# Performance work log

Hardware: AMD Instinct MI355X
Metric: run time of the kernel (lower is better)

The kernel has to match this reference:

```python
import jax, jax.numpy as jnp
import numpy as np

B, D, R = 256, 4096, 16
MAX_R = 2 * R - 1  # static upper bound on radius; per-row steps masked by r_mask


def setup_inputs() -> dict:
    key = jax.random.key(0)
    kx, kw, kb = jax.random.split(key, 3)
    x = (jax.random.uniform(kx, (B, D)) < 0.5).astype(jnp.float32)  # random bits
    A = jax.random.normal(kw, (D, D), dtype=jnp.float32) * 0.01
    W = (A + A.T) * 0.5  # symmetric quadratic coupling
    bias = jax.random.normal(kb, (D,), dtype=jnp.float32) * 0.1
    return {"x": x, "W": W, "bias": bias}


def reference(x, W, bias):
    # energy model: score(x) = 0.5 * x' W x + b' x  (per batch row)
    score_fn = lambda z: 0.5 * jnp.einsum('bd,de,be->b', z, W, z) + z @ bias
    grad_fn = jax.grad(lambda z: score_fn(z).sum())

    key = jax.random.key(42)
    k_rad, k_samp, k_acc = jax.random.split(key, 3)
    radius = jax.random.randint(k_rad, (B, 1), 1, 2 * R)
    r_mask = (jnp.arange(MAX_R)[None, :] < radius).astype(x.dtype)  # [B, MAX_R]

    score_x = score_fn(x)                                  # [B]
    grad_x = jax.lax.stop_gradient(grad_fn(x))             # detach as in torch
    score_change_x = (1.0 - 2.0 * x) * grad_x * 0.5        # [B, D] proposal logits

    b_idx = jnp.arange(B)

    def body(carry, inp):
        cur_x, blocked = carry
        k, m = inp  # per-step RNG key, per-step mask column [B]
        idx = jax.random.categorical(k, score_change_x + blocked)  # multinomial w/ zeroed probs
        cur_bits = cur_x[b_idx, idx]
        cur_x = cur_x.at[b_idx, idx].set(m * (1.0 - cur_bits) + (1.0 - m) * cur_bits)
        blocked = blocked.at[b_idx, idx].set(-jnp.inf)  # prob_x[b, idx] = 0
        return (cur_x, blocked), idx

    keys = jax.random.split(k_samp, MAX_R)
    (y, _), idx_steps = jax.lax.scan(body, (x, jnp.zeros_like(x)), (keys, r_mask.T))
    idx_all = idx_steps.T  # [B, MAX_R]

    score_y = score_fn(y)
    grad_y = jax.lax.stop_gradient(grad_fn(y))
    score_change_y = (1.0 - 2.0 * y) * grad_y * 0.5

    # masked log-softmax tensors: step j's proposal excludes indices flipped at other steps
    oh = jax.nn.one_hot(idx_all, D, dtype=x.dtype)        # [B, MAX_R, D]
    cum = jnp.cumsum(oh, axis=1)
    before = cum - oh                                      # indices sampled at steps i < j
    after = cum[:, -1:, :] - cum                           # indices sampled at steps i > j
    change_fwd = jnp.where(before > 0, -jnp.inf, score_change_x[:, None, :])
    change_bwd = jnp.where(after > 0, -jnp.inf, score_change_y[:, None, :])

    g_fwd = jnp.take_along_axis(jax.nn.log_softmax(change_fwd, axis=-1), idx_all[:, :, None], axis=2)[..., 0]
    g_bwd = jnp.take_along_axis(jax.nn.log_softmax(change_bwd, axis=-1), idx_all[:, :, None], axis=2)[..., 0]
    log_fwd = jnp.sum(g_fwd * r_mask, axis=-1) + score_x
    log_bwd = jnp.sum(g_bwd * r_mask, axis=-1) + score_y

    log_acc = log_bwd - log_fwd
    u = jax.random.uniform(k_acc, (B,))
    accepted = (jnp.exp(log_acc) >= u).astype(x.dtype)[:, None]  # [B, 1]
    y_sg = jax.lax.stop_gradient(y)
    acc_sg = jax.lax.stop_gradient(accepted)
    return y_sg * acc_sg + (1.0 - acc_sg) * x
```

## Files before the change

### kernel.cpp

```cpp
#include <hip/hip_runtime.h>
#include <math.h>

#define BB 256
#define DD 4096
#define MAXR 31
#define NCAND 4
#define CAPG 192
#define U_THRESH 0.9778f
#define GUARD 4.0f

typedef unsigned short u16;
typedef u16 u16x4 __attribute__((ext_vector_type(4)));
typedef u16 u16x8 __attribute__((ext_vector_type(8)));
typedef __bf16 bf16x8 __attribute__((ext_vector_type(8)));
typedef float f32x16 __attribute__((ext_vector_type(16)));

__device__ __forceinline__ void tf2x32(unsigned k0, unsigned k1, unsigned c0, unsigned c1,
                                       unsigned &o0, unsigned &o1) {
  unsigned ks2 = k0 ^ k1 ^ 0x1BD11BDAu;
  unsigned x0 = c0 + k0;
  unsigned x1 = c1 + k1;
#define TF_ROT(v, r) (((v) << (r)) | ((v) >> (32 - (r))))
#define TF_R(r) { x0 += x1; x1 = TF_ROT(x1, r); x1 ^= x0; }
  TF_R(13) TF_R(15) TF_R(26) TF_R(6)   x0 += k1;  x1 += ks2 + 1u;
  TF_R(17) TF_R(29) TF_R(16) TF_R(24)  x0 += ks2; x1 += k0 + 2u;
  TF_R(13) TF_R(15) TF_R(26) TF_R(6)   x0 += k0;  x1 += k1 + 3u;
  TF_R(17) TF_R(29) TF_R(16) TF_R(24)  x0 += k1;  x1 += ks2 + 4u;
  TF_R(13) TF_R(15) TF_R(26) TF_R(6)   x0 += ks2; x1 += k0 + 5u;
#undef TF_R
#undef TF_ROT
  o0 = x0; o1 = x1;
}

__device__ __forceinline__ unsigned tf_xor(unsigned k0, unsigned k1, unsigned c0, unsigned c1) {
  unsigned a, b; tf2x32(k0, k1, c0, c1, a, b); return a ^ b;
}

__device__ __forceinline__ float bits_to_unit(unsigned bits) {
  return __uint_as_float(0x3f800000u | (bits >> 9)) - 1.0f;
}

__device__ __forceinline__ void keys_of(int j, unsigned &kk0, unsigned &kk1) {
  unsigned ks0, ks1;
  tf2x32(0u, 42u, 0u, 1u, ks0, ks1);
  tf2x32(ks0, ks1, 0u, (unsigned)j, kk0, kk1);
}

__device__ __forceinline__ int radius_of(int b) {
  unsigned krad0, krad1, k10, k11, k20, k21;
  tf2x32(0u, 42u, 0u, 0u, krad0, krad1);
  tf2x32(krad0, krad1, 0u, 0u, k10, k11);
  tf2x32(krad0, krad1, 0u, 1u, k20, k21);
  unsigned hi = tf_xor(k10, k11, 0u, (unsigned)b);
  unsigned lo = tf_xor(k20, k21, 0u, (unsigned)b);
  return 1 + (int)(((hi % 31u) * 4u + (lo % 31u)) % 31u);
}

__device__ __forceinline__ float uacc_of(int b) {
  unsigned ka0, ka1;
  tf2x32(0u, 42u, 0u, 2u, ka0, ka1);
  return bits_to_unit(tf_xor(ka0, ka1, 0u, (unsigned)b));
}

__device__ __forceinline__ double dlog(double x) {
  unsigned long long ub = (unsigned long long)__double_as_longlong(x);
  int e = (int)((ub >> 52) & 0x7FFull) - 1022;
  double m = __longlong_as_double((long long)((ub & 0x000FFFFFFFFFFFFFull) | 0x3FE0000000000000ull));
  if (m < 0.70710678118654752440) { m *= 2.0; e -= 1; }
  double r = (m - 1.0) / (m + 1.0);
  double z = r * r;
  double s = fma(z, fma(z, fma(z, fma(z, fma(z, fma(z, 1.0/15.0, 1.0/13.0),
                1.0/11.0), 1.0/9.0), 1.0/7.0), 1.0/5.0), 1.0/3.0);
  double t2 = 2.0 * r;
  return fma((double)e, 0.69314718055994530942, fma(t2 * z, s, t2));
}

__device__ __forceinline__ float gumbel_from_u(float f) {
  float uu = (f == 0.0f) ? 1.17549435e-38f : f;
  float t1 = (float)dlog((double)uu);
  return -(float)dlog((double)(-t1));
}

__device__ __forceinline__ float gumbel_of(unsigned kk0, unsigned kk1, unsigned n) {
  return gumbel_from_u(bits_to_unit(tf_xor(kk0, kk1, 0u, n)));
}

__device__ __forceinline__ double blockReduce1024(double v, double* lds) {
  int t = threadIdx.x;
  #pragma unroll
  for (int off = 32; off > 0; off >>= 1) v += __shfl_down(v, off);
  __syncthreads();
  if ((t & 63) == 0) lds[t >> 6] = v;
  __syncthreads();
  double s = 0.0;
  #pragma unroll
  for (int i = 0; i < 16; i++) s += lds[i];
  return s;
}

__device__ __forceinline__ void split3(float w, u16 &h, u16 &l, u16 &q) {
  __bf16 hb = (__bf16)w;
  float r = w - (float)hb;
  __bf16 lb = (__bf16)r;
  float r2 = r - (float)lb;
  __bf16 qb = (__bf16)r2;
  h = __builtin_bit_cast(u16, hb);
  l = __builtin_bit_cast(u16, lb);
  q = __builtin_bit_cast(u16, qb);
}

__global__ __launch_bounds__(256, 2) void k_mega(
    const float* __restrict__ x, const float* __restrict__ W,
    float* __restrict__ Cpart, int klen, int ngemm,
    u16* __restrict__ flt_list, int* __restrict__ flt_cnt) {
  int t = threadIdx.x;

  if ((int)blockIdx.x < ngemm) {
    int g = blockIdx.x;
    int nt = g & 63, mt = (g >> 6) & 1, kc = g >> 7;
    int k0 = kc * klen;

    __shared__ alignas(16) u16 As[4][128][8];
    __shared__ alignas(16) u16 Bs[3][4][64][8];

    const float* xrow = x + (size_t)(mt * 128) * DD + k0;
    const float* wrow = W + (size_t)(nt * 64) * DD + k0;

    int am = t >> 2, akg = t & 3;
    int bn = t >> 2, bkg = t & 3;

    float4 aR0, aR1, aR2, aR3;
    float4 bR0, bR1;
    int nsteps = klen / 32;

    {
      const float* ap = xrow + (size_t)am * DD + akg * 8;
      aR0 = *(const float4*)ap;       aR1 = *(const float4*)(ap + 4);
      const float* ap2 = ap + (size_t)64 * DD;
      aR2 = *(const float4*)ap2;      aR3 = *(const float4*)(ap2 + 4);
      const float* wp = wrow + (size_t)bn * DD + bkg * 8;
      bR0 = *(const float4*)wp;       bR1 = *(const float4*)(wp + 4);
    }

    int wid = t >> 6, lane = t & 63;
    int wr = (wid >> 1) * 64, wc = (wid & 1) * 32;
    int lm = lane & 31, lh = lane >> 5;

    f32x16 acc[2];
    #pragma unroll
    for (int i = 0; i < 2; i++)
      #pragma unroll
      for (int r = 0; r < 16; r++) acc[i][r] = 0.0f;

    for (int s = 0; s < nsteps; s++) {
      __syncthreads();
      {
        float af32[8];
        *(float4*)&af32[0] = aR0; *(float4*)&af32[4] = aR1;
        u16x8 av;
        #pragma unroll
        for (int i = 0; i < 8; i++) av[i] = __builtin_bit_cast(u16, (__bf16)af32[i]);
        *(u16x8*)&As[akg][am][0] = av;
        *(float4*)&af32[0] = aR2; *(float4*)&af32[4] = aR3;
        #pragma unroll
        for (int i = 0; i < 8; i++) av[i] = __builtin_bit_cast(u16, (__bf16)af32[i]);
        *(u16x8*)&As[akg][am + 64][0] = av;
      }
      {
        float wv[8];
        *(float4*)&wv[0] = bR0; *(float4*)&wv[4] = bR1;
        u16x8 ph, pl, pq;
        #pragma unroll
        for (int i = 0; i < 8; i++) {
          u16 hh, ll, qq;
          split3(wv[i], hh, ll, qq);
          ph[i] = hh; pl[i] = ll; pq[i] = qq;
        }
        *(u16x8*)&Bs[0][bkg][bn][0] = ph;
        *(u16x8*)&Bs[1][bkg][bn][0] = pl;
        *(u16x8*)&Bs[2][bkg][bn][0] = pq;
      }
      __syncthreads();
      if (s + 1 < nsteps) {
        int kk = (s + 1) * 32;
        const float* ap = xrow + (size_t)am * DD + kk + akg * 8;
        aR0 = *(const float4*)ap;       aR1 = *(const float4*)(ap + 4);
        const float* ap2 = ap + (size_t)64 * DD;
        aR2 = *(const float4*)ap2;      aR3 = *(const float4*)(ap2 + 4);
        const float* wp = wrow + (size_t)bn * DD + kk + bkg * 8;
        bR0 = *(const float4*)wp;       bR1 = *(const float4*)(wp + 4);
      }
      bf16x8 af[2][2];
      #pragma unroll
      for (int mf = 0; mf < 2; mf++)
        #pragma unroll
        for (int h = 0; h < 2; h++)
          af[mf][h] = *(const bf16x8*)&As[2 * h + lh][wr + mf * 32 + lm][0];
      __builtin_amdgcn_s_setprio(1);
      #pragma unroll
      for (int p = 0; p < 3; p++) {
        bf16x8 b0 = *(const bf16x8*)&Bs[p][lh][wc + lm][0];
        bf16x8 b1 = *(const bf16x8*)&Bs[p][2 + lh][wc + lm][0];
        #pragma unroll
        for (int mf = 0; mf < 2; mf++) {
          acc[mf] = __builtin_amdgcn_mfma_f32_32x32x16_bf16(af[mf][0], b0, acc[mf], 0, 0, 0);
          acc[mf] = __builtin_amdgcn_mfma_f32_32x32x16_bf16(af[mf][1], b1, acc[mf], 0, 0, 0);
        }
      }
      __builtin_amdgcn_s_setprio(0);
    }

    float* Cp = Cpart + (size_t)kc * ((size_t)BB * DD);
    #pragma unroll
    for (int mf = 0; mf < 2; mf++) {
      int col   = nt * 64 + wc + lm;
      int rbase = mt * 128 + wr + mf * 32 + 4 * lh;
      #pragma unroll
      for (int r = 0; r < 16; r++) {
        int row = rbase + (r & 3) + 8 * (r >> 2);
        Cp[(size_t)row * DD + col] = acc[mf][r];
      }
    }
  } else {
    int fb = (int)blockIdx.x - ngemm;
    int b = fb / MAXR, j = fb % MAXR;
    unsigned kk0, kk1;
    keys_of(j, kk0, kk1);
    unsigned base = (unsigned)(b * DD);

    __shared__ int fcnt;
    __shared__ u16 fl[CAPG];
    if (t == 0) fcnt = 0;
    __syncthreads();

    #pragma unroll
    for (int p = 0; p < 16; p++) {
      int d = t + 256*p;
      unsigned bits = tf_xor(kk0, kk1, 0u, base + (unsigned)d);
      float f = bits_to_unit(bits);
      if (f >= U_THRESH) {
        int pos = atomicAdd(&fcnt, 1);
        if (pos < CAPG) fl[pos] = (u16)d;
      }
    }
    __syncthreads();
    int n = fcnt;
    if (t == 0) flt_cnt[fb] = n;
    int nstore = n < CAPG ? n : CAPG;
    if (t < nstore) flt_list[(size_t)fb * CAPG + t] = fl[t];
  }
}

__global__ __launch_bounds__(1024) void k_redscore(
    const float* __restrict__ Cpart, const float* __restrict__ bias,
    const float* __restrict__ x, float* __restrict__ grad, float* __restrict__ sc,
    double* __restrict__ score, float* __restrict__ scmax, int KS) {
  int b = blockIdx.x, t = threadIdx.x;
  int d0 = t * 4;
  size_t o = (size_t)b * DD + d0;
  float a0 = 0.f, a1 = 0.f, a2 = 0.f, a3 = 0.f;
  for (int kc = 0; kc < KS; kc++) {
    float4 c = *(const float4*)&Cpart[(size_t)kc * BB * DD + o];
    a0 += c.x; a1 += c.y; a2 += c.z; a3 += c.w;
  }
  float4 bv = *(const float4*)&bias[d0];
  float4 xv = *(const float4*)&x[o];
  float gg[4] = { a0 + bv.x, a1 + bv.y, a2 + bv.z, a3 + bv.w };
  float xx[4] = { xv.x, xv.y, xv.z, xv.w };
  float bb[4] = { bv.x, bv.y, bv.z, bv.w };
  *(float4*)&grad[o] = *(float4*)&gg[0];
  float scv[4];
  double s1 = 0.0, s2 = 0.0;
  float mx = -INFINITY;
  #pragma unroll
  for (int k = 0; k < 4; k++) {
    scv[k] = (1.0f - 2.0f * xx[k]) * gg[k] * 0.5f;
    mx = fmaxf(mx, scv[k]);
    s1 += (double)xx[k] * (double)gg[k];
    s2 += (double)xx[k] * (double)bb[k];
  }
  *(float4*)&sc[o] = *(float4*)&scv[0];
  __shared__ double lds[16];
  double S1 = blockReduce1024(s1, lds);
  double S2 = blockReduce1024(s2, lds);
  #pragma unroll
  for (int off = 32; off > 0; off >>= 1) mx = fmaxf(mx, __shfl_down(mx, off));
  __shared__ float lmx[16];
  __syncthreads();
  if ((t & 63) == 0) lmx[t >> 6] = mx;
  __syncthreads();
  if (t == 0) {
    float m = lmx[0];
    #pragma unroll
    for (int i = 1; i < 16; i++) m = fmaxf(m, lmx[i]);
    score[b] = 0.5 * (S1 + S2);
    scmax[b] = m;
  }
}

__global__ __launch_bounds__(256) void k_topk(const float* __restrict__ sc_x,
                                              const float* __restrict__ scmax,
                                              const u16* __restrict__ flt_list,
                                              const int* __restrict__ flt_cnt,
                                              int* __restrict__ cand_i) {
  int fb = blockIdx.x;
  int b = fb / MAXR, j = fb % MAXR;
  unsigned kk0, kk1;
  keys_of(j, kk0, kk1);
  int t = threadIdx.x;
  unsigned base = (unsigned)(b * DD);

  __shared__ float win_v_s;
  __shared__ int   win_i_s;
  __shared__ float ls_v[4];
  __shared__ int   ls_i[4];

  int n = flt_cnt[fb];
  bool need_fallback = (n > CAPG) || (n < NCAND);

  if (!need_fallback) {
    float v; int di;
    if (t < n) {
      int d = (int)flt_list[(size_t)fb * CAPG + t];
      float f = bits_to_unit(tf_xor(kk0, kk1, 0u, base + (unsigned)d));
      v = sc_x[(size_t)b*DD + d] + gumbel_from_u(f);
      di = d;
    } else { v = -INFINITY; di = 0x7FFFFFFF; }
    bool dead = (t >= n);
    float v4 = -INFINITY;
    for (int r = 0; r < NCAND; r++) {
      float bv = dead ? -INFINITY : v;
      int   bi = dead ? 0x7FFFFFFF : di;
      #pragma unroll
      for (int off = 32; off > 0; off >>= 1) {
        float ov = __shfl_down(bv, off);
        int   oi = __shfl_down(bi, off);
        if (ov > bv || (ov == bv && oi < bi)) { bv = ov; bi = oi; }
      }
      if ((t & 63) == 0) { ls_v[t >> 6] = bv; ls_i[t >> 6] = bi; }
      __syncthreads();
      if (t == 0) {
        float fv = ls_v[0]; int fi = ls_i[0];
        #pragma unroll
        for (int w = 1; w < 4; w++)
          if (ls_v[w] > fv || (ls_v[w] == fv && ls_i[w] < fi)) { fv = ls_v[w]; fi = ls_i[w]; }
        win_v_s = fv; win_i_s = fi;
        cand_i[(size_t)fb * NCAND + r] = fi;
      }
      __syncthreads();
      v4 = win_v_s;
      if (di == win_i_s) dead = true;
    }
    if (v4 >= scmax[b] + GUARD) return;
    need_fallback = true;
    __syncthreads();
  }

  {
    float v[16];
    #pragma unroll
    for (int p = 0; p < 16; p++) {
      int d = t + 256*p;
      v[p] = sc_x[(size_t)b*DD + d] + gumbel_of(kk0, kk1, base + (unsigned)d);
    }
    unsigned alive = 0xFFFFu;
    float lv = -INFINITY; int li = 0x7FFFFFFF;
    #pragma unroll
    for (int p = 0; p < 16; p++)
      if (v[p] > lv) { lv = v[p]; li = t + 256*p; }
    for (int r = 0; r < NCAND; r++) {
      float bv = lv; int bi = li;
      #pragma unroll
      for (int off = 32; off > 0; off >>= 1) {
        float ov = __shfl_down(bv, off);
        int   oi = __shfl_down(bi, off);
        if (ov > bv || (ov == bv && oi < bi)) { bv = ov; bi = oi; }
      }
      if ((t & 63) == 0) { ls_v[t >> 6] = bv; ls_i[t >> 6] = bi; }
      __syncthreads();
      if (t == 0) {
        float fv = ls_v[0]; int fi = ls_i[0];
        #pragma unroll
        for (int w = 1; w < 4; w++)
          if (ls_v[w] > fv || (ls_v[w] == fv && ls_i[w] < fi)) { fv = ls_v[w]; fi = ls_i[w]; }
        win_i_s = fi;
        cand_i[(size_t)fb * NCAND + r] = fi;
      }
      __syncthreads();
      if (r < NCAND - 1) {
        int wi = win_i_s;
        if (t == (wi & 255)) {
          alive &= ~(1u << (wi >> 8));
          lv = -INFINITY; li = 0x7FFFFFFF;
          #pragma unroll
          for (int p = 0; p < 16; p++)
            if (((alive >> p) & 1u) && v[p] > lv) { lv = v[p]; li = t + 256*p; }
        }
      }
    }
  }
}

__global__ __launch_bounds__(1024) void k_sely(
    const int* __restrict__ cand_i, const float* __restrict__ sc_x,
    const float* __restrict__ x, const float* __restrict__ W,
    const float* __restrict__ bias, const float* __restrict__ grad_x,
    int* __restrict__ idx_all, float* __restrict__ yv, float* __restrict__ sc_y,
    double* __restrict__ score_y) {
  int b = blockIdx.x, t = threadIdx.x;
  __shared__ unsigned mask[128];
  __shared__ int cl[MAXR * NCAND];
  __shared__ int fidx[MAXR];
  __shared__ float fsgn[MAXR];
  __shared__ int jfail_s;
  __shared__ int nf_s;
  __shared__ float ls_v[16];
  __shared__ int   ls_i[16];
  if (t < 128) mask[t] = 0u;
  if (t < MAXR * NCAND) cl[t] = cand_i[(size_t)b * MAXR * NCAND + t];
  if (t == 0) nf_s = radius_of(b);
  __syncthreads();

  int jdone = 0;
  while (true) {
    if (t == 0) {
      int j = jdone;
      while (j < MAXR) {
        int pick = -1;
        #pragma unroll
        for (int r = 0; r < NCAND; r++) {
          int idx = cl[j * NCAND + r];
          if (pick < 0 && !((mask[idx >> 5] >> (idx & 31)) & 1u)) pick = idx;
        }
        if (pick < 0) break;
        fidx[j] = pick;
        idx_all[b * MAXR + j] = pick;
        mask[pick >> 5] |= (1u << (pick & 31));
        j++;
      }
      jfail_s = j;
    }
    __syncthreads();
    int jf = jfail_s;
    if (jf >= MAXR) break;
    {
      unsigned kk0, kk1;
      keys_of(jf, kk0, kk1);
      float lv = -INFINITY; int li = 0x7FFFFFFF;
      #pragma unroll
      for (int q = 0; q < 4; q++) {
        int d = t * 4 + q;
        if ((mask[d >> 5] >> (d & 31)) & 1u) continue;
        float vv = sc_x[(size_t)b*DD + d] + gumbel_of(kk0, kk1, (unsigned)(b*DD + d));
        if (vv > lv || (vv == lv && d < li)) { lv = vv; li = d; }
      }
      #pragma unroll
      for (int off = 32; off > 0; off >>= 1) {
        float ov = __shfl_down(lv, off);
        int   oi = __shfl_down(li, off);
        if (ov > lv || (ov == lv && oi < li)) { lv = ov; li = oi; }
      }
      if ((t & 63) == 0) { ls_v[t >> 6] = lv; ls_i[t >> 6] = li; }
      __syncthreads();
      if (t == 0) {
        float fv = ls_v[0]; int fi = ls_i[0];
        #pragma unroll
        for (int w = 1; w < 16; w++)
          if (ls_v[w] > fv || (ls_v[w] == fv && ls_i[w] < fi)) { fv = ls_v[w]; fi = ls_i[w]; }
        fidx[jf] = fi;
        idx_all[b * MAXR + jf] = fi;
        mask[fi >> 5] |= (1u << (fi & 31));
      }
      __syncthreads();
    }
    jdone = jf + 1;
  }

  int nf = nf_s;
  if (t < nf) fsgn[t] = 1.0f - 2.0f * x[(size_t)b*DD + fidx[t]];
  __syncthreads();

  int d0 = t * 4;
  size_t o = (size_t)b * DD + d0;
  float4 gv4 = *(const float4*)&grad_x[o];
  float4 xv4 = *(const float4*)&x[o];
  float4 bv4 = *(const float4*)&bias[d0];
  float g[4]  = { gv4.x, gv4.y, gv4.z, gv4.w };
  float xx[4] = { xv4.x, xv4.y, xv4.z, xv4.w };
  float yy[4] = { xv4.x, xv4.y, xv4.z, xv4.w };
  for (int jj = 0; jj < nf; jj++) {
    int fd = fidx[jj];
    float s = fsgn[jj];
    float4 wv = *(const float4*)&W[(size_t)fd * DD + d0];
    g[0] = fmaf(s, wv.x, g[0]);
    g[1] = fmaf(s, wv.y, g[1]);
    g[2] = fmaf(s, wv.z, g[2]);
    g[3] = fmaf(s, wv.w, g[3]);
    int r = fd - d0;
    if (r >= 0 && r < 4) yy[r] = 1.0f - xx[r];
  }
  float scy[4];
  double s1 = 0.0, s2 = 0.0;
  float bb[4] = { bv4.x, bv4.y, bv4.z, bv4.w };
  #pragma unroll
  for (int k = 0; k < 4; k++) {
    scy[k] = (1.0f - 2.0f * yy[k]) * g[k] * 0.5f;
    s1 += (double)yy[k] * (double)g[k];
    s2 += (double)yy[k] * (double)bb[k];
  }
  *(float4*)&yv[o]   = *(float4*)&yy[0];
  *(float4*)&sc_y[o] = *(float4*)&scy[0];
  __shared__ double lds[16];
  double S1 = blockReduce1024(s1, lds);
  double S2 = blockReduce1024(s2, lds);
  if (t == 0) score_y[b] = 0.5 * (S1 + S2);
}

__global__ __launch_bounds__(1024) void k_accept(
    const float* __restrict__ x, const float* __restrict__ yv,
    const float* __restrict__ sc_x, const float* __restrict__ sc_y,
    const int* __restrict__ idx_all,
    const double* __restrict__ score_x, const double* __restrict__ score_y,
    float* __restrict__ out) {
  int b = blockIdx.x, t = threadIdx.x;
  __shared__ float scx_s[MAXR], scy_s[MAXR];
  __shared__ int nf_s;
  if (t < MAXR) {
    int id = idx_all[b*MAXR + t];
    scx_s[t] = sc_x[(size_t)b*DD + id];
    scy_s[t] = sc_y[(size_t)b*DD + id];
  }
  if (t == 0) nf_s = radius_of(b);

  int d0 = t * 4;
  size_t o = (size_t)b * DD + d0;
  float4 sxv = *(const float4*)&sc_x[o];
  float4 syv = *(const float4*)&sc_y[o];
  double sx = exp((double)sxv.x) + exp((double)sxv.y) + exp((double)sxv.z) + exp((double)sxv.w);
  double sy = exp((double)syv.x) + exp((double)syv.y) + exp((double)syv.z) + exp((double)syv.w);
  __shared__ double lds[16];
  double S = blockReduce1024(sx, lds);
  double T = blockReduce1024(sy, lds);
  __shared__ float accf;
  __syncthreads();
  if (t < 32) {
    int nf = nf_s;
    int lane = t;
    double ex = (t < MAXR) ? exp((double)scx_s[t]) : 0.0;
    double scn = ex;
    #pragma unroll
    for (int off = 1; off < 32; off <<= 1) {
      double ov = __shfl_up(scn, off);
      if (lane >= off) scn += ov;
    }
    double pre = scn - ex;
    double gf = (t < nf) ? ((double)scx_s[t] - dlog(S - pre)) : 0.0;
    double ey = (t < MAXR) ? exp((double)scy_s[t]) : 0.0;
    double scn2 = ey;
    #pragma unroll
    for (int off = 1; off < 32; off <<= 1) {
      double ov = __shfl_down(scn2, off);
      if (lane + off < 32) scn2 += ov;
    }
    double suf = scn2 - ey;
    double gb = (t < nf) ? ((double)scy_s[t] - dlog(T - suf)) : 0.0;
    #pragma unroll
    for (int off = 16; off > 0; off >>= 1) {
      gf += __shfl_down(gf, off);
      gb += __shfl_down(gb, off);
    }
    if (t == 0) {
      double log_acc = (gb + score_y[b]) - (gf + score_x[b]);
      accf = (exp(log_acc) >= (double)uacc_of(b)) ? 1.0f : 0.0f;
    }
  }
  __syncthreads();
  float a = accf;
  float4 yv4 = *(const float4*)&yv[o];
  float4 xv4 = *(const float4*)&x[o];
  float4 ov4;
  ov4.x = a * yv4.x + (1.0f - a) * xv4.x;
  ov4.y = a * yv4.y + (1.0f - a) * xv4.y;
  ov4.z = a * yv4.z + (1.0f - a) * xv4.z;
  ov4.w = a * yv4.w + (1.0f - a) * xv4.w;
  *(float4*)&out[o] = ov4;
}

extern "C" void kernel_launch(void* const* d_in, const int* in_sizes, int n_in,
                              void* d_out, int out_size, void* d_ws, size_t ws_size,
                              hipStream_t stream) {
  const float* x    = (const float*)d_in[0];
  const float* W    = (const float*)d_in[1];
  const float* bias = (const float*)d_in[2];
  float* out = (float*)d_out;
  char* ws = (char*)d_ws;
  const size_t MB = 1ull << 20;
  const size_t KB = 1024;

  float*    grad_x   = (float*)   (ws + 0*MB);
  float*    sc_x     = (float*)   (ws + 4*MB);
  float*    sc_y     = (float*)   (ws + 8*MB);
  float*    yv       = (float*)   (ws + 12*MB);
  u16*      flt_list = (u16*)     (ws + 16*MB);
  int*      flt_cnt  = (int*)     (ws + 19*MB + 0*KB);
  int*      cand_i   = (int*)     (ws + 19*MB + 32*KB);
  int*      idx_all  = (int*)     (ws + 19*MB + 160*KB);
  double*   score_x  = (double*)  (ws + 19*MB + 192*KB);
  double*   score_y  = (double*)  (ws + 19*MB + 196*KB);
  float*    scmax    = (float*)   (ws + 19*MB + 200*KB);
  float*    Cpart    = (float*)   (ws + 20*MB);

  size_t base = 20*MB;
  int KS = 1;
  if      (ws_size >= base + 16*MB) KS = 4;
  else if (ws_size >= base +  8*MB) KS = 2;

  int NG = 64 * 2 * KS;

  k_mega    <<<NG + BB*MAXR, 256, 0, stream>>>(x, W, Cpart, DD/KS, NG, flt_list, flt_cnt);
  k_redscore<<<BB, 1024, 0, stream>>>(Cpart, bias, x, grad_x, sc_x, score_x, scmax, KS);
  k_topk    <<<BB*MAXR, 256, 0, stream>>>(sc_x, scmax, flt_list, flt_cnt, cand_i);
  k_sely    <<<BB, 1024, 0, stream>>>(cand_i, sc_x, x, W, bias, grad_x, idx_all, yv, sc_y, score_y);
  k_accept  <<<BB, 1024, 0, stream>>>(x, yv, sc_x, sc_y, idx_all, score_x, score_y, out);
}
```

Measured before the change: 254.7 us.

## Fuse score reduction, top-k, selection and acceptance into one per-row tail kernel

Merges the four post-GEMM kernels (redscore, topk, sely, accept) into a single 1024-thread block per batch row. The block keeps the proposal logits and gradient in shared memory, so the grad_x, sc_x, sc_y and yv arrays no longer round-trip through global memory. The 31 per-step candidate searches now run four at a time in 256-thread groups, where previously each step had its own block. The filter test also compares integer mantissa bits against a threshold instead of converting to float. The cost is that the 7936 top-k blocks collapse into 256 large blocks, which lowers parallelism and adds shared-memory pressure and serial per-row work.

After: 239.5 us. -6.0%, faster.

```diff
diff --git a/kernel.cpp b/kernel.cpp
--- a/kernel.cpp
+++ b/kernel.cpp
@@ -10,7 +10,6 @@
 #define GUARD 4.0f
 
 typedef unsigned short u16;
-typedef u16 u16x4 __attribute__((ext_vector_type(4)));
 typedef u16 u16x8 __attribute__((ext_vector_type(8)));
 typedef __bf16 bf16x8 __attribute__((ext_vector_type(8)));
 typedef float f32x16 __attribute__((ext_vector_type(16)));
@@ -226,7 +225,8 @@
     int b = fb / MAXR, j = fb % MAXR;
     unsigned kk0, kk1;
     keys_of(j, kk0, kk1);
-    unsigned base = (unsigned)(b * DD);
+    unsigned base_c = (unsigned)(b * DD);
+    const unsigned KMIN = (unsigned)ceil((double)U_THRESH * 8388608.0);
 
     __shared__ int fcnt;
     __shared__ u16 fl[CAPG];
@@ -235,10 +235,9 @@
 
     #pragma unroll
     for (int p = 0; p < 16; p++) {
-      int d = t + 256*p;
-      unsigned bits = tf_xor(kk0, kk1, 0u, base + (unsigned)d);
-      float f = bits_to_unit(bits);
-      if (f >= U_THRESH) {
+      int d = t + 256 * p;
+      unsigned bits = tf_xor(kk0, kk1, 0u, base_c + (unsigned)d);
+      if ((bits >> 9) >= KMIN) {
         int pos = atomicAdd(&fcnt, 1);
         if (pos < CAPG) fl[pos] = (u16)d;
       }
@@ -251,11 +250,34 @@
   }
 }
 
-__global__ __launch_bounds__(1024) void k_redscore(
+__global__ __launch_bounds__(1024) void k_tail(
     const float* __restrict__ Cpart, const float* __restrict__ bias,
-    const float* __restrict__ x, float* __restrict__ grad, float* __restrict__ sc,
-    double* __restrict__ score, float* __restrict__ scmax, int KS) {
+    const float* __restrict__ x, const float* __restrict__ W,
+    const u16* __restrict__ flt_list, const int* __restrict__ flt_cnt,
+    float* __restrict__ out, int KS) {
   int b = blockIdx.x, t = threadIdx.x;
+
+  __shared__ float sc_lds[DD];
+  __shared__ float gr_lds[DD];
+  __shared__ double redbuf[16];
+  __shared__ float lmx[16];
+  __shared__ float ls_v[16];
+  __shared__ int   ls_i[16];
+  __shared__ float win_v[4];
+  __shared__ int   win_i[4];
+  __shared__ int   cand_lds[MAXR][NCAND];
+  __shared__ int   fb_list[MAXR];
+  __shared__ int   nfb_s;
+  __shared__ int   fidx[MAXR];
+  __shared__ float fsgn[MAXR];
+  __shared__ unsigned mask[DD / 32];
+  __shared__ int   pick_s;
+  __shared__ int   nf_s;
+  __shared__ float scmax_s;
+  __shared__ double score_x_s, score_y_s, Ssum_s, Tsum_s;
+  __shared__ float scx_s[MAXR], scy_s[MAXR];
+  __shared__ float accf;
+
   int d0 = t * 4;
   size_t o = (size_t)b * DD + d0;
   float a0 = 0.f, a1 = 0.f, a2 = 0.f, a3 = 0.f;
@@ -263,12 +285,11 @@
     float4 c = *(const float4*)&Cpart[(size_t)kc * BB * DD + o];
     a0 += c.x; a1 += c.y; a2 += c.z; a3 += c.w;
   }
-  float4 bv = *(const float4*)&bias[d0];
-  float4 xv = *(const float4*)&x[o];
-  float gg[4] = { a0 + bv.x, a1 + bv.y, a2 + bv.z, a3 + bv.w };
-  float xx[4] = { xv.x, xv.y, xv.z, xv.w };
-  float bb[4] = { bv.x, bv.y, bv.z, bv.w };
-  *(float4*)&grad[o] = *(float4*)&gg[0];
+  float4 bv4 = *(const float4*)&bias[d0];
+  float4 xv4 = *(const float4*)&x[o];
+  float gg[4] = { a0 + bv4.x, a1 + bv4.y, a2 + bv4.z, a3 + bv4.w };
+  float xx[4] = { xv4.x, xv4.y, xv4.z, xv4.w };
+  float bb[4] = { bv4.x, bv4.y, bv4.z, bv4.w };
   float scv[4];
   double s1 = 0.0, s2 = 0.0;
   float mx = -INFINITY;
@@ -279,13 +300,16 @@
     s1 += (double)xx[k] * (double)gg[k];
     s2 += (double)xx[k] * (double)bb[k];
   }
-  *(float4*)&sc[o] = *(float4*)&scv[0];
-  __shared__ double lds[16];
-  double S1 = blockReduce1024(s1, lds);
-  double S2 = blockReduce1024(s2, lds);
+  *(float4*)&sc_lds[d0] = *(float4*)&scv[0];
+  *(float4*)&gr_lds[d0] = *(float4*)&gg[0];
+  if (t < 128) mask[t] = 0u;
+  if (t == 0) { nf_s = radius_of(b); nfb_s = 0; }
+  double sx = exp((double)scv[0]) + exp((double)scv[1]) + exp((double)scv[2]) + exp((double)scv[3]);
+  double S1 = blockReduce1024(s1, redbuf);
+  double S2 = blockReduce1024(s2, redbuf);
+  double Sv = blockReduce1024(sx, redbuf);
   #pragma unroll
   for (int off = 32; off > 0; off >>= 1) mx = fmaxf(mx, __shfl_down(mx, off));
-  __shared__ float lmx[16];
   __syncthreads();
   if ((t & 63) == 0) lmx[t >> 6] = mx;
   __syncthreads();
@@ -293,40 +317,33 @@
     float m = lmx[0];
     #pragma unroll
     for (int i = 1; i < 16; i++) m = fmaxf(m, lmx[i]);
-    score[b] = 0.5 * (S1 + S2);
-    scmax[b] = m;
-  }
-}
-
-__global__ __launch_bounds__(256) void k_topk(const float* __restrict__ sc_x,
-                                              const float* __restrict__ scmax,
-                                              const u16* __restrict__ flt_list,
-                                              const int* __restrict__ flt_cnt,
-                                              int* __restrict__ cand_i) {
-  int fb = blockIdx.x;
-  int b = fb / MAXR, j = fb % MAXR;
-  unsigned kk0, kk1;
-  keys_of(j, kk0, kk1);
-  int t = threadIdx.x;
-  unsigned base = (unsigned)(b * DD);
-
-  __shared__ float win_v_s;
-  __shared__ int   win_i_s;
-  __shared__ float ls_v[4];
-  __shared__ int   ls_i[4];
-
-  int n = flt_cnt[fb];
-  bool need_fallback = (n > CAPG) || (n < NCAND);
-
-  if (!need_fallback) {
-    float v; int di;
-    if (t < n) {
-      int d = (int)flt_list[(size_t)fb * CAPG + t];
-      float f = bits_to_unit(tf_xor(kk0, kk1, 0u, base + (unsigned)d));
-      v = sc_x[(size_t)b*DD + d] + gumbel_from_u(f);
+    score_x_s = 0.5 * (S1 + S2);
+    scmax_s = m;
+    Ssum_s = Sv;
+  }
+  __syncthreads();
+
+  int g = t >> 8, tg = t & 255;
+  float scmax_l = scmax_s;
+  for (int jj = 0; jj < 8; jj++) {
+    int j = jj * 4 + g;
+    bool active = (j < MAXR);
+    unsigned kk0 = 0, kk1 = 0;
+    int n = 0;
+    if (active) {
+      keys_of(j, kk0, kk1);
+      n = flt_cnt[b * MAXR + j];
+    }
+    bool fastok = active && !(n > CAPG || n < NCAND);
+    float v = -INFINITY; int di = 0x7FFFFFFF;
+    bool dead = true;
+    if (fastok && tg < n) {
+      int d = (int)flt_list[(size_t)(b * MAXR + j) * CAPG + tg];
+      float f = bits_to_unit(tf_xor(kk0, kk1, 0u, (unsigned)(b * DD) + (unsigned)d));
+      v = sc_lds[d] + gumbel_from_u(f);
       di = d;
-    } else { v = -INFINITY; di = 0x7FFFFFFF; }
-    bool dead = (t >= n);
+      dead = false;
+    }
     float v4 = -INFINITY;
     for (int r = 0; r < NCAND; r++) {
       float bv = dead ? -INFINITY : v;
@@ -339,87 +356,68 @@
       }
       if ((t & 63) == 0) { ls_v[t >> 6] = bv; ls_i[t >> 6] = bi; }
       __syncthreads();
+      if (tg == 0 && fastok) {
+        float fv = ls_v[4 * g]; int fi = ls_i[4 * g];
+        #pragma unroll
+        for (int w = 1; w < 4; w++)
+          if (ls_v[4 * g + w] > fv || (ls_v[4 * g + w] == fv && ls_i[4 * g + w] < fi)) { fv = ls_v[4 * g + w]; fi = ls_i[4 * g + w]; }
+        win_v[g] = fv; win_i[g] = fi;
+        cand_lds[j][r] = fi;
+      }
+      __syncthreads();
+      if (fastok) {
+        v4 = win_v[g];
+        if (di == win_i[g]) dead = true;
+      }
+    }
+    if (active && tg == 0) {
+      bool needfb = !fastok || (v4 < scmax_l + GUARD);
+      if (needfb) fb_list[atomicAdd(&nfb_s, 1)] = j;
+    }
+    __syncthreads();
+  }
+
+  int nfb = nfb_s;
+  for (int fi = 0; fi < nfb; fi++) {
+    int j = fb_list[fi];
+    unsigned kk0, kk1;
+    keys_of(j, kk0, kk1);
+    float vq[4]; int dq[4];
+    unsigned alive = 0xFu;
+    #pragma unroll
+    for (int q = 0; q < 4; q++) {
+      int d = t * 4 + q;
+      vq[q] = sc_lds[d] + gumbel_of(kk0, kk1, (unsigned)(b * DD + d));
+      dq[q] = d;
+    }
+    for (int r = 0; r < NCAND; r++) {
+      float lv = -INFINITY; int li = 0x7FFFFFFF;
+      #pragma unroll
+      for (int q = 0; q < 4; q++)
+        if (((alive >> q) & 1u) && (vq[q] > lv || (vq[q] == lv && dq[q] < li))) { lv = vq[q]; li = dq[q]; }
+      #pragma unroll
+      for (int off = 32; off > 0; off >>= 1) {
+        float ov = __shfl_down(lv, off);
+        int   oi = __shfl_down(li, off);
+        if (ov > lv || (ov == lv && oi < li)) { lv = ov; li = oi; }
+      }
+      if ((t & 63) == 0) { ls_v[t >> 6] = lv; ls_i[t >> 6] = li; }
+      __syncthreads();
       if (t == 0) {
-        float fv = ls_v[0]; int fi = ls_i[0];
-        #pragma unroll
-        for (int w = 1; w < 4; w++)
-          if (ls_v[w] > fv || (ls_v[w] == fv && ls_i[w] < fi)) { fv = ls_v[w]; fi = ls_i[w]; }
-        win_v_s = fv; win_i_s = fi;
-        cand_i[(size_t)fb * NCAND + r] = fi;
-      }
-      __syncthreads();
-      v4 = win_v_s;
-      if (di == win_i_s) dead = true;
-    }
-    if (v4 >= scmax[b] + GUARD) return;
-    need_fallback = true;
+        float fv = ls_v[0]; int fi2 = ls_i[0];
+        #pragma unroll
+        for (int w = 1; w < 16; w++)
+          if (ls_v[w] > fv || (ls_v[w] == fv && ls_i[w] < fi2)) { fv = ls_v[w]; fi2 = ls_i[w]; }
+        cand_lds[j][r] = fi2;
+        win_i[0] = fi2;
+      }
+      __syncthreads();
+      int wi = win_i[0];
+      #pragma unroll
+      for (int q = 0; q < 4; q++) if (dq[q] == wi) alive &= ~(1u << q);
+    }
     __syncthreads();
   }
-
-  {
-    float v[16];
-    #pragma unroll
-    for (int p = 0; p < 16; p++) {
-      int d = t + 256*p;
-      v[p] = sc_x[(size_t)b*DD + d] + gumbel_of(kk0, kk1, base + (unsigned)d);
-    }
-    unsigned alive = 0xFFFFu;
-    float lv = -INFINITY; int li = 0x7FFFFFFF;
-    #pragma unroll
-    for (int p = 0; p < 16; p++)
-      if (v[p] > lv) { lv = v[p]; li = t + 256*p; }
-    for (int r = 0; r < NCAND; r++) {
-      float bv = lv; int bi = li;
-      #pragma unroll
-      for (int off = 32; off > 0; off >>= 1) {
-        float ov = __shfl_down(bv, off);
-        int   oi = __shfl_down(bi, off);
-        if (ov > bv || (ov == bv && oi < bi)) { bv = ov; bi = oi; }
-      }
-      if ((t & 63) == 0) { ls_v[t >> 6] = bv; ls_i[t >> 6] = bi; }
-      __syncthreads();
-      if (t == 0) {
-        float fv = ls_v[0]; int fi = ls_i[0];
-        #pragma unroll
-        for (int w = 1; w < 4; w++)
-          if (ls_v[w] > fv || (ls_v[w] == fv && ls_i[w] < fi)) { fv = ls_v[w]; fi = ls_i[w]; }
-        win_i_s = fi;
-        cand_i[(size_t)fb * NCAND + r] = fi;
-      }
-      __syncthreads();
-      if (r < NCAND - 1) {
-        int wi = win_i_s;
-        if (t == (wi & 255)) {
-          alive &= ~(1u << (wi >> 8));
-          lv = -INFINITY; li = 0x7FFFFFFF;
-          #pragma unroll
-          for (int p = 0; p < 16; p++)
-            if (((alive >> p) & 1u) && v[p] > lv) { lv = v[p]; li = t + 256*p; }
-        }
-      }
-    }
-  }
-}
-
-__global__ __launch_bounds__(1024) void k_sely(
-    const int* __restrict__ cand_i, const float* __restrict__ sc_x,
-    const float* __restrict__ x, const float* __restrict__ W,
-    const float* __restrict__ bias, const float* __restrict__ grad_x,
-    int* __restrict__ idx_all, float* __restrict__ yv, float* __restrict__ sc_y,
-    double* __restrict__ score_y) {
-  int b = blockIdx.x, t = threadIdx.x;
-  __shared__ unsigned mask[128];
-  __shared__ int cl[MAXR * NCAND];
-  __shared__ int fidx[MAXR];
-  __shared__ float fsgn[MAXR];
-  __shared__ int jfail_s;
-  __shared__ int nf_s;
-  __shared__ float ls_v[16];
-  __shared__ int   ls_i[16];
-  if (t < 128) mask[t] = 0u;
-  if (t < MAXR * NCAND) cl[t] = cand_i[(size_t)b * MAXR * NCAND + t];
-  if (t == 0) nf_s = radius_of(b);
-  __syncthreads();
 
   int jdone = 0;
   while (true) {
@@ -429,19 +427,18 @@
         int pick = -1;
         #pragma unroll
         for (int r = 0; r < NCAND; r++) {
-          int idx = cl[j * NCAND + r];
+          int idx = cand_lds[j][r];
           if (pick < 0 && !((mask[idx >> 5] >> (idx & 31)) & 1u)) pick = idx;
         }
         if (pick < 0) break;
         fidx[j] = pick;
-        idx_all[b * MAXR + j] = pick;
         mask[pick >> 5] |= (1u << (pick & 31));
         j++;
       }
-      jfail_s = j;
+      pick_s = j;
     }
     __syncthreads();
-    int jf = jfail_s;
+    int jf = pick_s;
     if (jf >= MAXR) break;
     {
       unsigned kk0, kk1;
@@ -451,7 +448,7 @@
       for (int q = 0; q < 4; q++) {
         int d = t * 4 + q;
         if ((mask[d >> 5] >> (d & 31)) & 1u) continue;
-        float vv = sc_x[(size_t)b*DD + d] + gumbel_of(kk0, kk1, (unsigned)(b*DD + d));
+        float vv = sc_lds[d] + gumbel_of(kk0, kk1, (unsigned)(b * DD + d));
         if (vv > lv || (vv == lv && d < li)) { lv = vv; li = d; }
       }
       #pragma unroll
@@ -463,13 +460,12 @@
       if ((t & 63) == 0) { ls_v[t >> 6] = lv; ls_i[t >> 6] = li; }
       __syncthreads();
       if (t == 0) {
-        float fv = ls_v[0]; int fi = ls_i[0];
+        float fv = ls_v[0]; int fi2 = ls_i[0];
         #pragma unroll
         for (int w = 1; w < 16; w++)
-          if (ls_v[w] > fv || (ls_v[w] == fv && ls_i[w] < fi)) { fv = ls_v[w]; fi = ls_i[w]; }
-        fidx[jf] = fi;
-        idx_all[b * MAXR + jf] = fi;
-        mask[fi >> 5] |= (1u << (fi & 31));
+          if (ls_v[w] > fv || (ls_v[w] == fv && ls_i[w] < fi2)) { fv = ls_v[w]; fi2 = ls_i[w]; }
+        fidx[jf] = fi2;
+        mask[fi2 >> 5] |= (1u << (fi2 & 31));
       }
       __syncthreads();
     }
@@ -477,75 +473,48 @@
   }
 
   int nf = nf_s;
-  if (t < nf) fsgn[t] = 1.0f - 2.0f * x[(size_t)b*DD + fidx[t]];
-  __syncthreads();
-
-  int d0 = t * 4;
-  size_t o = (size_t)b * DD + d0;
-  float4 gv4 = *(const float4*)&grad_x[o];
-  float4 xv4 = *(const float4*)&x[o];
-  float4 bv4 = *(const float4*)&bias[d0];
-  float g[4]  = { gv4.x, gv4.y, gv4.z, gv4.w };
-  float xx[4] = { xv4.x, xv4.y, xv4.z, xv4.w };
-  float yy[4] = { xv4.x, xv4.y, xv4.z, xv4.w };
+  if (t < nf) fsgn[t] = 1.0f - 2.0f * x[(size_t)b * DD + fidx[t]];
+  __syncthreads();
+
+  float gd[4] = { gr_lds[d0], gr_lds[d0 + 1], gr_lds[d0 + 2], gr_lds[d0 + 3] };
+  float yy[4] = { xx[0], xx[1], xx[2], xx[3] };
   for (int jj = 0; jj < nf; jj++) {
     int fd = fidx[jj];
     float s = fsgn[jj];
     float4 wv = *(const float4*)&W[(size_t)fd * DD + d0];
-    g[0] = fmaf(s, wv.x, g[0]);
-    g[1] = fmaf(s, wv.y, g[1]);
-    g[2] = fmaf(s, wv.z, g[2]);
-    g[3] = fmaf(s, wv.w, g[3]);
+    gd[0] = fmaf(s, wv.x, gd[0]);
+    gd[1] = fmaf(s, wv.y, gd[1]);
+    gd[2] = fmaf(s, wv.z, gd[2]);
+    gd[3] = fmaf(s, wv.w, gd[3]);
     int r = fd - d0;
     if (r >= 0 && r < 4) yy[r] = 1.0f - xx[r];
   }
   float scy[4];
-  double s1 = 0.0, s2 = 0.0;
-  float bb[4] = { bv4.x, bv4.y, bv4.z, bv4.w };
+  double t1 = 0.0, t2 = 0.0;
   #pragma unroll
   for (int k = 0; k < 4; k++) {
-    scy[k] = (1.0f - 2.0f * yy[k]) * g[k] * 0.5f;
-    s1 += (double)yy[k] * (double)g[k];
-    s2 += (double)yy[k] * (double)bb[k];
-  }
-  *(float4*)&yv[o]   = *(float4*)&yy[0];
-  *(float4*)&sc_y[o] = *(float4*)&scy[0];
-  __shared__ double lds[16];
-  double S1 = blockReduce1024(s1, lds);
-  double S2 = blockReduce1024(s2, lds);
-  if (t == 0) score_y[b] = 0.5 * (S1 + S2);
-}
-
-__global__ __launch_bounds__(1024) void k_accept(
-    const float* __restrict__ x, const float* __restrict__ yv,
-    const float* __restrict__ sc_x, const float* __restrict__ sc_y,
-    const int* __restrict__ idx_all,
-    const double* __restrict__ score_x, const double* __restrict__ score_y,
-    float* __restrict__ out) {
-  int b = blockIdx.x, t = threadIdx.x;
-  __shared__ float scx_s[MAXR], scy_s[MAXR];
-  __shared__ int nf_s;
+    scy[k] = (1.0f - 2.0f * yy[k]) * gd[k] * 0.5f;
+    t1 += (double)yy[k] * (double)gd[k];
+    t2 += (double)yy[k] * (double)bb[k];
+  }
+  double sy = exp((double)scy[0]) + exp((double)scy[1]) + exp((double)scy[2]) + exp((double)scy[3]);
+  __syncthreads();
+  *(float4*)&gr_lds[d0] = *(float4*)&scy[0];
+  double T1 = blockReduce1024(t1, redbuf);
+  double T2 = blockReduce1024(t2, redbuf);
+  double Tv = blockReduce1024(sy, redbuf);
+  if (t == 0) { score_y_s = 0.5 * (T1 + T2); Tsum_s = Tv; }
+  __syncthreads();
+
   if (t < MAXR) {
-    int id = idx_all[b*MAXR + t];
-    scx_s[t] = sc_x[(size_t)b*DD + id];
-    scy_s[t] = sc_y[(size_t)b*DD + id];
-  }
-  if (t == 0) nf_s = radius_of(b);
-
-  int d0 = t * 4;
-  size_t o = (size_t)b * DD + d0;
-  float4 sxv = *(const float4*)&sc_x[o];
-  float4 syv = *(const float4*)&sc_y[o];
-  double sx = exp((double)sxv.x) + exp((double)sxv.y) + exp((double)sxv.z) + exp((double)sxv.w);
-  double sy = exp((double)syv.x) + exp((double)syv.y) + exp((double)syv.z) + exp((double)syv.w);
-  __shared__ double lds[16];
-  double S = blockReduce1024(sx, lds);
-  double T = blockReduce1024(sy, lds);
-  __shared__ float accf;
+    int id = fidx[t];
+    scx_s[t] = sc_lds[id];
+    scy_s[t] = gr_lds[id];
+  }
   __syncthreads();
   if (t < 32) {
-    int nf = nf_s;
     int lane = t;
+    double S = Ssum_s, T = Tsum_s;
     double ex = (t < MAXR) ? exp((double)scx_s[t]) : 0.0;
     double scn = ex;
     #pragma unroll
@@ -570,19 +539,17 @@
       gb += __shfl_down(gb, off);
     }
     if (t == 0) {
-      double log_acc = (gb + score_y[b]) - (gf + score_x[b]);
+      double log_acc = (gb + score_y_s) - (gf + score_x_s);
       accf = (exp(log_acc) >= (double)uacc_of(b)) ? 1.0f : 0.0f;
     }
   }
   __syncthreads();
   float a = accf;
-  float4 yv4 = *(const float4*)&yv[o];
-  float4 xv4 = *(const float4*)&x[o];
   float4 ov4;
-  ov4.x = a * yv4.x + (1.0f - a) * xv4.x;
-  ov4.y = a * yv4.y + (1.0f - a) * xv4.y;
-  ov4.z = a * yv4.z + (1.0f - a) * xv4.z;
-  ov4.w = a * yv4.w + (1.0f - a) * xv4.w;
+  ov4.x = a * yy[0] + (1.0f - a) * xx[0];
+  ov4.y = a * yy[1] + (1.0f - a) * xx[1];
+  ov4.z = a * yy[2] + (1.0f - a) * xx[2];
+  ov4.w = a * yy[3] + (1.0f - a) * xx[3];
   *(float4*)&out[o] = ov4;
 }
 
@@ -595,31 +562,18 @@
   float* out = (float*)d_out;
   char* ws = (char*)d_ws;
   const size_t MB = 1ull << 20;
-  const size_t KB = 1024;
-
-  float*    grad_x   = (float*)   (ws + 0*MB);
-  float*    sc_x     = (float*)   (ws + 4*MB);
-  float*    sc_y     = (float*)   (ws + 8*MB);
-  float*    yv       = (float*)   (ws + 12*MB);
-  u16*      flt_list = (u16*)     (ws + 16*MB);
-  int*      flt_cnt  = (int*)     (ws + 19*MB + 0*KB);
-  int*      cand_i   = (int*)     (ws + 19*MB + 32*KB);
-  int*      idx_all  = (int*)     (ws + 19*MB + 160*KB);
-  double*   score_x  = (double*)  (ws + 19*MB + 192*KB);
-  double*   score_y  = (double*)  (ws + 19*MB + 196*KB);
-  float*    scmax    = (float*)   (ws + 19*MB + 200*KB);
-  float*    Cpart    = (float*)   (ws + 20*MB);
-
-  size_t base = 20*MB;
+
+  u16*    flt_list = (u16*)(ws + 0*MB);
+  int*    flt_cnt  = (int*)(ws + 3*MB);
+  float*  Cpart    = (float*)(ws + 4*MB);
+
+  size_t base = 4*MB;
   int KS = 1;
   if      (ws_size >= base + 16*MB) KS = 4;
   else if (ws_size >= base +  8*MB) KS = 2;
 
   int NG = 64 * 2 * KS;
 
-  k_mega    <<<NG + BB*MAXR, 256, 0, stream>>>(x, W, Cpart, DD/KS, NG, flt_list, flt_cnt);
-  k_redscore<<<BB, 1024, 0, stream>>>(Cpart, bias, x, grad_x, sc_x, score_x, scmax, KS);
-  k_topk    <<<BB*MAXR, 256, 0, stream>>>(sc_x, scmax, flt_list, flt_cnt, cand_i);
-  k_sely    <<<BB, 1024, 0, stream>>>(cand_i, sc_x, x, W, bias, grad_x, idx_all, yv, sc_y, score_y);
-  k_accept  <<<BB, 1024, 0, stream>>>(x, yv, sc_x, sc_y, idx_all, score_x, score_y, out);
-}
+  k_mega<<<NG + BB*MAXR, 256, 0, stream>>>(x, W, Cpart, DD/KS, NG, flt_list, flt_cnt);
+  k_tail<<<BB, 1024, 0, stream>>>(Cpart, bias, x, W, flt_list, flt_cnt, out, KS);
+}
```
